# Kernel optimization log

Hardware: AMD Instinct MI355X
Metric: run time of the kernel (lower is better)

Reference implementation:

```python
import jax, jax.numpy as jnp
import numpy as np

N = 768          # number of atoms
DIM = 3
F = 128          # feature width
N_RBF = 32       # gaussian radial basis size
CUTOFF = 5.0
NUM_CHAINS = 4
T_IN_K = 300.0
TTIME = 20.0
KB = 8.617330337217213e-05   # Boltzmann constant, eV/K (ASE units.kB)
BOX = 24.8                   # box side so that ~26 neighbors/atom within cutoff
GAMMA = 1.0 / (CUTOFF / N_RBF) ** 2  # RBF width


def setup_inputs() -> dict:
    key = jax.random.key(0)
    ks = jax.random.split(key, 12)
    q = jax.random.uniform(ks[0], (N, DIM), dtype=jnp.float32) * BOX
    v = jax.random.normal(ks[1], (N, DIM), dtype=jnp.float32) * 0.01
    p_eta = jax.random.normal(ks[2], (NUM_CHAINS,), dtype=jnp.float32) * 0.1
    mass = jax.random.uniform(ks[3], (N,), dtype=jnp.float32, minval=1.0, maxval=20.0)
    atomic_numbers = jax.random.randint(ks[4], (N,), 0, 100, dtype=jnp.int32)
    embed = jax.random.normal(ks[5], (100, F), dtype=jnp.float32) * 0.1
    W1 = jax.random.normal(ks[6], (N_RBF, F), dtype=jnp.float32) / np.sqrt(N_RBF)
    b1 = jnp.zeros((F,), dtype=jnp.float32)
    W2 = jax.random.normal(ks[7], (F, F), dtype=jnp.float32) / np.sqrt(F)
    b2 = jnp.zeros((F,), dtype=jnp.float32)
    W3 = jax.random.normal(ks[8], (F, F), dtype=jnp.float32) / np.sqrt(F)
    w_out = jax.random.normal(ks[9], (F,), dtype=jnp.float32) / np.sqrt(F)
    return dict(v=v, q=q, p_eta=p_eta, mass=mass, embed=embed, W1=W1, b1=b1,
                W2=W2, b2=b2, W3=W3, w_out=w_out, atomic_numbers=atomic_numbers)


def _energy(q, atomic_numbers, embed, W1, b1, W2, b2, W3, w_out):
    """SchNet-style cutoff-graph potential energy (scalar)."""
    h = embed[atomic_numbers]                                   # [N,F]
    disp = q[:, None, :] - q[None, :, :]                        # [N,N,3]
    d2 = jnp.sum(disp * disp, axis=-1)                          # [N,N]
    eye = jnp.eye(N, dtype=bool)
    mask = (d2 < CUTOFF ** 2) & (~eye)                          # cutoff neighbor list (dense mask)
    d = jnp.sqrt(jnp.where(mask, d2, 1.0))                      # safe sqrt off-graph
    centers = jnp.linspace(0.0, CUTOFF, N_RBF, dtype=q.dtype)
    rbf = jnp.exp(-GAMMA * (d[..., None] - centers) ** 2)       # [N,N,n_rbf]
    filt = jax.nn.relu(rbf @ W1 + b1) @ W2 + b2                 # [N,N,F]
    filt = jnp.where(mask[..., None], filt, 0.0)
    m = jnp.einsum('ijf,jf->if', filt, h)                       # message aggregation
    h = h + jax.nn.relu(m @ W3)
    return jnp.sum(h @ w_out)


def reference(v, q, p_eta, mass, embed, W1, b1, W2, b2, W3, w_out, atomic_numbers):
    kT = T_IN_K * KB
    n_dof = N * DIM
    target_ke = 0.5 * n_dof * kT
    Q = 2.0 * jnp.array([n_dof * kT * TTIME ** 2] + [kT * TTIME ** 2] * (NUM_CHAINS - 1),
                        dtype=v.dtype)
    p = v * mass[:, None]                                       # momenta
    current_ke = 0.5 * jnp.sum(p * p / mass[:, None])
    # f = -dE/dq (torch: -results['energy_grad'])
    f = -jax.grad(_energy)(q, atomic_numbers, embed, W1, b1, W2, b2, W3, w_out)
    coupled_forces = (p_eta[0] * p.reshape(-1) / Q[0]).reshape(-1, 3)
    dvdt = (f - coupled_forces) / mass[:, None]
    dpeta_first = 2.0 * (current_ke - target_ke) - p_eta[0] * p_eta[1] / Q[1]
    dpeta_mid = p_eta[:-2] ** 2 / Q[:-2] - kT - p_eta[1:-1] * p_eta[2:] / Q[2:]
    dpeta_last = p_eta[-2] ** 2 / Q[-2] - kT
    dpeta_dt = jnp.concatenate([dpeta_first[None], dpeta_mid, dpeta_last[None]])
    return (dvdt, v, dpeta_dt)
```

## Files before the change

kernel.cpp:

```cpp
#include <hip/hip_runtime.h>
#include <math.h>

#define N_ATOMS 768
#define FD 128
#define NRBF 32
#define MAXN 64
#define NTHREADS 512
#define TST 136
#define RSTU 40

constexpr float  CUT2   = 25.0f;
constexpr float  GAMMA_ = 40.96f;
constexpr float  CSTEP  = 5.0f / 31.0f;
constexpr double KB_D   = 8.617330337217213e-05;
constexpr double KT_D   = 300.0 * KB_D;
constexpr float  KT_F   = (float)KT_D;
constexpr float  TARGET_KE = (float)(0.5 * 2304.0 * KT_D);
constexpr float  Q0_F   = (float)(2.0 * 2304.0 * KT_D * 400.0);
constexpr float  QI_F   = (float)(2.0 * KT_D * 400.0);

#define DVDT_OFF 0
#define V_OFF    (3 * N_ATOMS)
#define PETA_OFF (6 * N_ATOMS)

using short8v = __attribute__((ext_vector_type(8))) short;
using f32x4   = __attribute__((ext_vector_type(4))) float;

#define MFMA_B16 __builtin_amdgcn_mfma_f32_16x16x32_bf16

__device__ __forceinline__ unsigned short f2bf(float x) {
    unsigned int u = __float_as_uint(x);
    u += 0x7FFF + ((u >> 16) & 1);
    return (unsigned short)(u >> 16);
}
__device__ __forceinline__ float bf2f(unsigned short h) {
    return __uint_as_float(((unsigned int)h) << 16);
}


__global__ __launch_bounds__(NTHREADS) void atom_kernel(
    const float* __restrict__ q,
    const float* __restrict__ W1, const float* __restrict__ b1,
    const float* __restrict__ W2, const float* __restrict__ b2,
    const float* __restrict__ embed, const int* __restrict__ z,
    const float* __restrict__ W3, const float* __restrict__ wout,
    float* __restrict__ f_acc)
{
    __shared__ int   nj[MAXN];
    __shared__ float nd[MAXN], ndx[MAXN], ndy[MAXN], ndz[MAXN];
    __shared__ int   cnt_s;
    __shared__ int   z_s[N_ATOMS];
    __shared__ __align__(16) unsigned short poolR[2 * MAXN * RSTU];
    __shared__ __align__(16) unsigned short poolA[2 * MAXN * TST];
    __shared__ float mrow[FD], gb[FD], mbrow[FD];
    __shared__ float sred[8 * MAXN];

    unsigned short* rbf_h  = poolR;
    unsigned short* rbf_l  = poolR + MAXN * RSTU;
    unsigned short* crbf_h = poolR;
    unsigned short* crbf_l = poolR + MAXN * RSTU;
    unsigned short* a1h  = poolA;
    unsigned short* a1l  = poolA + MAXN * TST;
    unsigned short* ts_h = poolA;
    unsigned short* ts_l = poolA + MAXN * TST;

    int i = blockIdx.x, t = threadIdx.x;
    int wid = t >> 6, lane = t & 63;
    int lr = lane & 15, lg = lane >> 4;
    int c0 = wid * 16 + lr;

    if (t == 0) cnt_s = 0;
    __syncthreads();

    float w1f32[8], w2ff32[4][8];
#pragma unroll
    for (int e = 0; e < 8; e++)
        w1f32[e] = W1[(lg * 8 + e) * FD + c0];
#pragma unroll
    for (int ks = 0; ks < 4; ks++)
#pragma unroll
        for (int e = 0; e < 8; e++)
            w2ff32[ks][e] = W2[(ks * 32 + lg * 8 + e) * FD + c0];
    float bb0  = b1[c0];
    float b2c0 = b2[c0];

    float qx = q[i*3], qy = q[i*3+1], qz = q[i*3+2];
    for (int j = t; j < N_ATOMS; j += NTHREADS) {
        z_s[j] = z[j];
        if (j == i) continue;
        float dx = qx - q[j*3], dy = qy - q[j*3+1], dz = qz - q[j*3+2];
        float d2 = dx*dx + dy*dy + dz*dz;
        if (d2 < CUT2) {
            int p = atomicAdd(&cnt_s, 1);
            if (p < MAXN) { nj[p] = j; nd[p] = sqrtf(d2);
                            ndx[p] = dx; ndy[p] = dy; ndz[p] = dz; }
        }
    }
    __syncthreads();
    int cnt = min(cnt_s, MAXN);
    if (cnt == 0) return;
    int ntl = (cnt + 15) >> 4;

    short8v w1h_r, w1l_r, w2f_h[4], w2f_l[4];
#pragma unroll
    for (int e = 0; e < 8; e++) {
        unsigned short hb = f2bf(w1f32[e]);
        w1h_r[e] = (short)hb;
        w1l_r[e] = (short)f2bf(w1f32[e] - bf2f(hb));
    }
#pragma unroll
    for (int ks = 0; ks < 4; ks++)
#pragma unroll
        for (int e = 0; e < 8; e++) {
            unsigned short hb = f2bf(w2ff32[ks][e]);
            w2f_h[ks][e] = (short)hb;
            w2f_l[ks][e] = (short)f2bf(w2ff32[ks][e] - bf2f(hb));
        }

    float macc0 = 0.f;
    unsigned int mk = 0;

    float4 hj0[2];
#pragma unroll
    for (int e = 0; e < 2; e++) {
        int idx = t + e * NTHREADS;
        int p = idx >> 5, c4g = (idx & 31) * 4;
        hj0[e] = (p < cnt)
            ? *(const float4*)(embed + z_s[nj[p]] * FD + c4g)
            : make_float4(0.f, 0.f, 0.f, 0.f);
    }

    for (int e = 0; e < ntl; e++) {
        int idx = t + e * NTHREADS;
        int p = idx >> 5, k = idx & 31;
        float d = (p < cnt) ? nd[p] : 1.0f;
        float u = d - CSTEP * (float)k;
        float r = __expf(-GAMMA_ * u * u);
        unsigned short hb = f2bf(r);
        rbf_h[p * RSTU + k] = hb;
        rbf_l[p * RSTU + k] = f2bf(r - bf2f(hb));
    }
    __syncthreads();

    for (int tl = 0; tl < ntl; tl++) {
        int rb = tl * 16;
        f32x4 u0 = {bb0, bb0, bb0, bb0};
        short8v rh = *(const short8v*)(rbf_h + (rb + lr) * RSTU + lg * 8);
        short8v rl = *(const short8v*)(rbf_l + (rb + lr) * RSTU + lg * 8);
        u0 = MFMA_B16(rh, w1h_r, u0, 0,0,0);
        u0 = MFMA_B16(rh, w1l_r, u0, 0,0,0);
        u0 = MFMA_B16(rl, w1h_r, u0, 0,0,0);
#pragma unroll
        for (int r = 0; r < 4; r++) {
            int p = rb + lg * 4 + r;
            if (u0[r] > 0.f) mk |= 1u << (4 * tl + r);
            float v = fmaxf(u0[r], 0.f);
            unsigned short hb = f2bf(v);
            a1h[p * TST + c0] = hb;
            a1l[p * TST + c0] = f2bf(v - bf2f(hb));
        }
    }
    __syncthreads();

    for (int tl = 0; tl < ntl; tl++) {
        int rb = tl * 16;
        float hv[4];
#pragma unroll
        for (int r = 0; r < 4; r++) {
            int p = rb + lg * 4 + r;
            hv[r] = (p < cnt) ? embed[z_s[nj[p]] * FD + c0] : 0.f;
        }
        f32x4 acc = {0.f, 0.f, 0.f, 0.f};
#pragma unroll
        for (int ks = 0; ks < 4; ks++) {
            int kb = ks * 32 + lg * 8;
            short8v ah = *(const short8v*)(a1h + (rb + lr) * TST + kb);
            short8v al = *(const short8v*)(a1l + (rb + lr) * TST + kb);
            acc = MFMA_B16(ah, w2f_h[ks], acc, 0,0,0);
            acc = MFMA_B16(ah, w2f_l[ks], acc, 0,0,0);
            acc = MFMA_B16(al, w2f_h[ks], acc, 0,0,0);
        }
#pragma unroll
        for (int r = 0; r < 4; r++) macc0 += (acc[r] + b2c0) * hv[r];
    }

    short8v w2b_h[4], w2b_l[4];
#pragma unroll
    for (int ks = 0; ks < 4; ks++) {
        int kb = ks * 32 + lg * 8;
        float4 a = *(const float4*)(W2 + c0 * FD + kb);
        float4 b = *(const float4*)(W2 + c0 * FD + kb + 4);
        float vv[8] = {a.x, a.y, a.z, a.w, b.x, b.y, b.z, b.w};
#pragma unroll
        for (int e = 0; e < 8; e++) {
            unsigned short hb = f2bf(vv[e]);
            w2b_h[ks][e] = (short)hb;
            w2b_l[ks][e] = (short)f2bf(vv[e] - bf2f(hb));
        }
    }

    {
        float r0 = macc0 + __shfl_xor(macc0, 16, 64);
        r0 += __shfl_xor(r0, 32, 64);
        if (lg == 0) mrow[c0] = r0;
    }
    __syncthreads();

    {
        int f0h = lg * 32;
        float g = 0.f;
#pragma unroll 8
        for (int f = f0h; f < f0h + 32; f++)
            g += mrow[f] * W3[f * FD + c0];
        g += __shfl_xor(g, 16, 64);
        g += __shfl_xor(g, 32, 64);
        if (lg == 0) gb[c0] = (g > 0.f) ? wout[c0] : 0.f;
    }
    __syncthreads();
    {
        int f0h = lg * 32;
        float mb = 0.f;
#pragma unroll
        for (int f4 = 0; f4 < 32; f4 += 4) {
            float4 w  = *(const float4*)(W3 + c0 * FD + f0h + f4);
            float4 gv = *(const float4*)(gb + f0h + f4);
            mb += gv.x*w.x + gv.y*w.y + gv.z*w.z + gv.w*w.w;
        }
        mb += __shfl_xor(mb, 16, 64);
        mb += __shfl_xor(mb, 32, 64);
        if (lg == 0) mbrow[c0] = mb;
    }
    __syncthreads();

    for (int e = 0; e < ntl; e++) {
        int idx = t + e * NTHREADS;
        int p = idx >> 5, k = idx & 31;
        float d = (p < cnt) ? nd[p] : 1.0f;
        float u = d - CSTEP * (float)k;
        float r = __expf(-GAMMA_ * u * u);
        float cd = -2.f * GAMMA_ * u * r;
        unsigned short hc = f2bf(cd);
        crbf_h[p * RSTU + k] = hc;
        crbf_l[p * RSTU + k] = f2bf(cd - bf2f(hc));
    }
    for (int e = 0; e < ntl; e++) {
        int idx = t + e * NTHREADS;
        int p = idx >> 5, c4g = (idx & 31) * 4;
        ushort4 hv = {0,0,0,0}, lv = {0,0,0,0};
        if (p < cnt) {
            float4 mb4 = *(const float4*)(mbrow + c4g);
            float4 hj4 = (e < 2) ? hj0[e]
                : *(const float4*)(embed + z_s[nj[p]] * FD + c4g);
            float v0 = mb4.x*hj4.x, v1 = mb4.y*hj4.y;
            float v2 = mb4.z*hj4.z, v3 = mb4.w*hj4.w;
            hv.x = f2bf(v0); lv.x = f2bf(v0 - bf2f(hv.x));
            hv.y = f2bf(v1); lv.y = f2bf(v1 - bf2f(hv.y));
            hv.z = f2bf(v2); lv.z = f2bf(v2 - bf2f(hv.z));
            hv.w = f2bf(v3); lv.w = f2bf(v3 - bf2f(hv.w));
        }
        *(ushort4*)(ts_h + p * TST + c4g) = hv;
        *(ushort4*)(ts_l + p * TST + c4g) = lv;
    }
    __syncthreads();

    for (int tl = 0; tl < ntl; tl++) {
        int rb = tl * 16;
        f32x4 ef = {0.f, 0.f, 0.f, 0.f};
        {
            short8v ch = *(const short8v*)(crbf_h + (rb + lr) * RSTU + lg * 8);
            short8v cl = *(const short8v*)(crbf_l + (rb + lr) * RSTU + lg * 8);
            ef = MFMA_B16(ch, w1h_r, ef, 0,0,0);
            ef = MFMA_B16(ch, w1l_r, ef, 0,0,0);
            ef = MFMA_B16(cl, w1h_r, ef, 0,0,0);
        }
        unsigned int mt = (mk >> (4 * tl)) & 0xFu;
#pragma unroll
        for (int r = 0; r < 4; r++)
            ef[r] = (mt & (1u << r)) ? ef[r] : 0.f;

        f32x4 acc = {0.f, 0.f, 0.f, 0.f};
#pragma unroll
        for (int ks = 0; ks < 4; ks++) {
            int kb = ks * 32 + lg * 8;
            short8v ah = *(const short8v*)(ts_h + (rb + lr) * TST + kb);
            short8v al = *(const short8v*)(ts_l + (rb + lr) * TST + kb);
            acc = MFMA_B16(ah, w2b_h[ks], acc, 0,0,0);
            acc = MFMA_B16(ah, w2b_l[ks], acc, 0,0,0);
            acc = MFMA_B16(al, w2b_h[ks], acc, 0,0,0);
        }

        float p4[4];
#pragma unroll
        for (int r = 0; r < 4; r++) p4[r] = acc[r] * ef[r];
#pragma unroll
        for (int mask = 1; mask < 16; mask <<= 1) {
#pragma unroll
            for (int e = 0; e < 4; e++) p4[e] += __shfl_xor(p4[e], mask, 64);
        }
        if (lr == 0) {
#pragma unroll
            for (int r = 0; r < 4; r++)
                sred[wid * MAXN + rb + lg * 4 + r] = p4[r];
        }
    }
    __syncthreads();

    float iax = 0.f, iay = 0.f, iaz = 0.f;
    if (t < MAXN && t < cnt) {
        float s = 0.f;
#pragma unroll
        for (int w = 0; w < 8; w++) s += sred[w * MAXN + t];
        float coef = s / nd[t];
        float fx = coef * ndx[t];
        float fy = coef * ndy[t];
        float fz = coef * ndz[t];
        iax = fx; iay = fy; iaz = fz;
        atomicAdd(f_acc + nj[t]*3 + 0, fx);
        atomicAdd(f_acc + nj[t]*3 + 1, fy);
        atomicAdd(f_acc + nj[t]*3 + 2, fz);
    }

    if (t < MAXN) {
#pragma unroll
        for (int mask = 1; mask < 64; mask <<= 1) {
            iax += __shfl_xor(iax, mask, 64);
            iay += __shfl_xor(iay, mask, 64);
            iaz += __shfl_xor(iaz, mask, 64);
        }
        if (t == 0) {
            atomicAdd(f_acc + i*3 + 0, -iax);
            atomicAdd(f_acc + i*3 + 1, -iay);
            atomicAdd(f_acc + i*3 + 2, -iaz);
        }
    }
}

__global__ __launch_bounds__(256) void fin_kernel(
    const float* __restrict__ v, const float* __restrict__ mass,
    const float* __restrict__ p_eta, const float* __restrict__ f_acc,
    float* __restrict__ out)
{
    __shared__ float red[256];
    int t = threadIdx.x;
    float ke = 0.f;
    float c = p_eta[0] / Q0_F;
    for (int idx = t; idx < 3 * N_ATOMS; idx += 256) {
        int a = idx / 3;
        float vv = v[idx], mi = mass[a];
        out[DVDT_OFF + idx] = (f_acc[idx] - c * vv * mi) / mi;
        out[V_OFF + idx] = vv;
        ke += 0.5f * mi * vv * vv;
    }
    red[t] = ke;
    __syncthreads();
    for (int s = 128; s > 0; s >>= 1) {
        if (t < s) red[t] += red[t + s];
        __syncthreads();
    }
    if (t == 0) {
        float k0 = red[0];
        float e0 = p_eta[0], e1 = p_eta[1], e2 = p_eta[2], e3 = p_eta[3];
        out[PETA_OFF + 0] = 2.f * (k0 - TARGET_KE) - e0 * e1 / QI_F;
        out[PETA_OFF + 1] = e0 * e0 / Q0_F - KT_F - e1 * e2 / QI_F;
        out[PETA_OFF + 2] = e1 * e1 / QI_F - KT_F - e2 * e3 / QI_F;
        out[PETA_OFF + 3] = e2 * e2 / QI_F - KT_F;
    }
}

extern "C" void kernel_launch(void* const* d_in, const int* in_sizes, int n_in,
                              void* d_out, int out_size, void* d_ws, size_t ws_size,
                              hipStream_t stream)
{
    const float* v     = (const float*)d_in[0];
    const float* q     = (const float*)d_in[1];
    const float* p_eta = (const float*)d_in[2];
    const float* mass  = (const float*)d_in[3];
    const float* embed = (const float*)d_in[4];
    const float* W1    = (const float*)d_in[5];
    const float* b1    = (const float*)d_in[6];
    const float* W2    = (const float*)d_in[7];
    const float* b2    = (const float*)d_in[8];
    const float* W3    = (const float*)d_in[9];
    const float* wout  = (const float*)d_in[10];
    const int*   z     = (const int*)d_in[11];
    float* out = (float*)d_out;

    float* f_acc = (float*)d_ws;

    hipMemsetAsync(f_acc, 0, 3 * N_ATOMS * sizeof(float), stream);

    atom_kernel<<<N_ATOMS, NTHREADS, 0, stream>>>(q, W1, b1, W2, b2,
                                                  embed, z, W3, wout, f_acc);
    fin_kernel<<<1, 256, 0, stream>>>(v, mass, p_eta, f_acc, out);
}
```

Baseline: 117.9 us.

## Process three atoms per block and prefetch next atom's neighbor list

The grid shrinks from one block per atom to 256 persistent blocks, each handling three atoms in sequence. The per-block weight loading and bf16 hi/lo splitting of W1/W2 now happens once for three atoms instead of once per atom. The neighbor search for the next atom runs in double-buffered shared arrays, interleaved with the current atom's work to hide its global loads. In exchange there are fewer blocks (256, roughly the CU count) and less parallelism to hide latency, so each block's three atoms run strictly one after another.

```diff
diff --git a/kernel.cpp b/kernel.cpp
--- a/kernel.cpp
+++ b/kernel.cpp
@@ -6,6 +6,7 @@
 #define NRBF 32
 #define MAXN 64
 #define NTHREADS 512
+#define NBLOCKS 256
 #define TST 136
 #define RSTU 40
 
@@ -46,9 +47,9 @@
     const float* __restrict__ W3, const float* __restrict__ wout,
     float* __restrict__ f_acc)
 {
-    __shared__ int   nj[MAXN];
-    __shared__ float nd[MAXN], ndx[MAXN], ndy[MAXN], ndz[MAXN];
-    __shared__ int   cnt_s;
+    __shared__ int   nj2[2][MAXN];
+    __shared__ float nd2[2][MAXN], ndx2[2][MAXN], ndy2[2][MAXN], ndz2[2][MAXN];
+    __shared__ int   cnt2[2];
     __shared__ int   z_s[N_ATOMS];
     __shared__ __align__(16) unsigned short poolR[2 * MAXN * RSTU];
     __shared__ __align__(16) unsigned short poolA[2 * MAXN * TST];
@@ -64,12 +65,12 @@
     unsigned short* ts_h = poolA;
     unsigned short* ts_l = poolA + MAXN * TST;
 
-    int i = blockIdx.x, t = threadIdx.x;
+    int b = blockIdx.x, t = threadIdx.x;
     int wid = t >> 6, lane = t & 63;
     int lr = lane & 15, lg = lane >> 4;
     int c0 = wid * 16 + lr;
 
-    if (t == 0) cnt_s = 0;
+    if (t < 2) cnt2[t] = 0;
     __syncthreads();
 
     float w1f32[8], w2ff32[4][8];
@@ -84,22 +85,20 @@
     float bb0  = b1[c0];
     float b2c0 = b2[c0];
 
-    float qx = q[i*3], qy = q[i*3+1], qz = q[i*3+2];
-    for (int j = t; j < N_ATOMS; j += NTHREADS) {
-        z_s[j] = z[j];
-        if (j == i) continue;
-        float dx = qx - q[j*3], dy = qy - q[j*3+1], dz = qz - q[j*3+2];
-        float d2 = dx*dx + dy*dy + dz*dz;
-        if (d2 < CUT2) {
-            int p = atomicAdd(&cnt_s, 1);
-            if (p < MAXN) { nj[p] = j; nd[p] = sqrtf(d2);
-                            ndx[p] = dx; ndy[p] = dy; ndz[p] = dz; }
-        }
-    }
-    __syncthreads();
-    int cnt = min(cnt_s, MAXN);
-    if (cnt == 0) return;
-    int ntl = (cnt + 15) >> 4;
+    {
+        float qx = q[b*3], qy = q[b*3+1], qz = q[b*3+2];
+        for (int j = t; j < N_ATOMS; j += NTHREADS) {
+            z_s[j] = z[j];
+            if (j == b) continue;
+            float dx = qx - q[j*3], dy = qy - q[j*3+1], dz = qz - q[j*3+2];
+            float d2 = dx*dx + dy*dy + dz*dz;
+            if (d2 < CUT2) {
+                int p = atomicAdd(&cnt2[0], 1);
+                if (p < MAXN) { nj2[0][p] = j; nd2[0][p] = sqrtf(d2);
+                                ndx2[0][p] = dx; ndy2[0][p] = dy; ndz2[0][p] = dz; }
+            }
+        }
+    }
 
     short8v w1h_r, w1l_r, w2f_h[4], w2f_l[4];
 #pragma unroll
@@ -116,81 +115,13 @@
             w2f_h[ks][e] = (short)hb;
             w2f_l[ks][e] = (short)f2bf(w2ff32[ks][e] - bf2f(hb));
         }
-
-    float macc0 = 0.f;
-    unsigned int mk = 0;
-
-    float4 hj0[2];
-#pragma unroll
-    for (int e = 0; e < 2; e++) {
-        int idx = t + e * NTHREADS;
-        int p = idx >> 5, c4g = (idx & 31) * 4;
-        hj0[e] = (p < cnt)
-            ? *(const float4*)(embed + z_s[nj[p]] * FD + c4g)
-            : make_float4(0.f, 0.f, 0.f, 0.f);
-    }
-
-    for (int e = 0; e < ntl; e++) {
-        int idx = t + e * NTHREADS;
-        int p = idx >> 5, k = idx & 31;
-        float d = (p < cnt) ? nd[p] : 1.0f;
-        float u = d - CSTEP * (float)k;
-        float r = __expf(-GAMMA_ * u * u);
-        unsigned short hb = f2bf(r);
-        rbf_h[p * RSTU + k] = hb;
-        rbf_l[p * RSTU + k] = f2bf(r - bf2f(hb));
-    }
-    __syncthreads();
-
-    for (int tl = 0; tl < ntl; tl++) {
-        int rb = tl * 16;
-        f32x4 u0 = {bb0, bb0, bb0, bb0};
-        short8v rh = *(const short8v*)(rbf_h + (rb + lr) * RSTU + lg * 8);
-        short8v rl = *(const short8v*)(rbf_l + (rb + lr) * RSTU + lg * 8);
-        u0 = MFMA_B16(rh, w1h_r, u0, 0,0,0);
-        u0 = MFMA_B16(rh, w1l_r, u0, 0,0,0);
-        u0 = MFMA_B16(rl, w1h_r, u0, 0,0,0);
-#pragma unroll
-        for (int r = 0; r < 4; r++) {
-            int p = rb + lg * 4 + r;
-            if (u0[r] > 0.f) mk |= 1u << (4 * tl + r);
-            float v = fmaxf(u0[r], 0.f);
-            unsigned short hb = f2bf(v);
-            a1h[p * TST + c0] = hb;
-            a1l[p * TST + c0] = f2bf(v - bf2f(hb));
-        }
-    }
-    __syncthreads();
-
-    for (int tl = 0; tl < ntl; tl++) {
-        int rb = tl * 16;
-        float hv[4];
-#pragma unroll
-        for (int r = 0; r < 4; r++) {
-            int p = rb + lg * 4 + r;
-            hv[r] = (p < cnt) ? embed[z_s[nj[p]] * FD + c0] : 0.f;
-        }
-        f32x4 acc = {0.f, 0.f, 0.f, 0.f};
-#pragma unroll
-        for (int ks = 0; ks < 4; ks++) {
-            int kb = ks * 32 + lg * 8;
-            short8v ah = *(const short8v*)(a1h + (rb + lr) * TST + kb);
-            short8v al = *(const short8v*)(a1l + (rb + lr) * TST + kb);
-            acc = MFMA_B16(ah, w2f_h[ks], acc, 0,0,0);
-            acc = MFMA_B16(ah, w2f_l[ks], acc, 0,0,0);
-            acc = MFMA_B16(al, w2f_h[ks], acc, 0,0,0);
-        }
-#pragma unroll
-        for (int r = 0; r < 4; r++) macc0 += (acc[r] + b2c0) * hv[r];
-    }
-
     short8v w2b_h[4], w2b_l[4];
 #pragma unroll
     for (int ks = 0; ks < 4; ks++) {
         int kb = ks * 32 + lg * 8;
-        float4 a = *(const float4*)(W2 + c0 * FD + kb);
-        float4 b = *(const float4*)(W2 + c0 * FD + kb + 4);
-        float vv[8] = {a.x, a.y, a.z, a.w, b.x, b.y, b.z, b.w};
+        float4 a4 = *(const float4*)(W2 + c0 * FD + kb);
+        float4 b4 = *(const float4*)(W2 + c0 * FD + kb + 4);
+        float vv[8] = {a4.x, a4.y, a4.z, a4.w, b4.x, b4.y, b4.z, b4.w};
 #pragma unroll
         for (int e = 0; e < 8; e++) {
             unsigned short hb = f2bf(vv[e]);
@@ -198,140 +129,236 @@
             w2b_l[ks][e] = (short)f2bf(vv[e] - bf2f(hb));
         }
     }
-
-    {
-        float r0 = macc0 + __shfl_xor(macc0, 16, 64);
-        r0 += __shfl_xor(r0, 32, 64);
-        if (lg == 0) mrow[c0] = r0;
-    }
     __syncthreads();
 
-    {
-        int f0h = lg * 32;
-        float g = 0.f;
+    for (int a = 0; a < 3; a++) {
+        int i   = b + NBLOCKS * a;
+        int buf = a & 1;
+        int nbuf = buf ^ 1;
+        int* njb = nj2[buf];
+        float* ndb = nd2[buf], *ndxb = ndx2[buf], *ndyb = ndy2[buf], *ndzb = ndz2[buf];
+
+        int cnt = min(cnt2[buf], MAXN);
+        int ntl = (cnt + 15) >> 4;
+        if (a < 2 && t == 0) cnt2[nbuf] = 0;
+
+        float macc0 = 0.f;
+        unsigned int mk = 0;
+
+        float4 hj0[2];
+#pragma unroll
+        for (int e = 0; e < 2; e++) {
+            int idx = t + e * NTHREADS;
+            int p = idx >> 5, c4g = (idx & 31) * 4;
+            hj0[e] = (p < cnt)
+                ? *(const float4*)(embed + z_s[njb[p]] * FD + c4g)
+                : make_float4(0.f, 0.f, 0.f, 0.f);
+        }
+
+        for (int e = 0; e < ntl; e++) {
+            int idx = t + e * NTHREADS;
+            int p = idx >> 5, k = idx & 31;
+            float d = (p < cnt) ? ndb[p] : 1.0f;
+            float u = d - CSTEP * (float)k;
+            float r = __expf(-GAMMA_ * u * u);
+            unsigned short hb = f2bf(r);
+            rbf_h[p * RSTU + k] = hb;
+            rbf_l[p * RSTU + k] = f2bf(r - bf2f(hb));
+        }
+        __syncthreads();
+
+        for (int tl = 0; tl < ntl; tl++) {
+            int rb = tl * 16;
+            f32x4 u0 = {bb0, bb0, bb0, bb0};
+            short8v rh = *(const short8v*)(rbf_h + (rb + lr) * RSTU + lg * 8);
+            short8v rl = *(const short8v*)(rbf_l + (rb + lr) * RSTU + lg * 8);
+            u0 = MFMA_B16(rh, w1h_r, u0, 0,0,0);
+            u0 = MFMA_B16(rh, w1l_r, u0, 0,0,0);
+            u0 = MFMA_B16(rl, w1h_r, u0, 0,0,0);
+#pragma unroll
+            for (int r = 0; r < 4; r++) {
+                int p = rb + lg * 4 + r;
+                if (u0[r] > 0.f) mk |= 1u << (4 * tl + r);
+                float v = fmaxf(u0[r], 0.f);
+                unsigned short hb = f2bf(v);
+                a1h[p * TST + c0] = hb;
+                a1l[p * TST + c0] = f2bf(v - bf2f(hb));
+            }
+        }
+        __syncthreads();
+
+        for (int tl = 0; tl < ntl; tl++) {
+            int rb = tl * 16;
+            float hv[4];
+#pragma unroll
+            for (int r = 0; r < 4; r++) {
+                int p = rb + lg * 4 + r;
+                hv[r] = (p < cnt) ? embed[z_s[njb[p]] * FD + c0] : 0.f;
+            }
+            f32x4 acc = {0.f, 0.f, 0.f, 0.f};
+#pragma unroll
+            for (int ks = 0; ks < 4; ks++) {
+                int kb = ks * 32 + lg * 8;
+                short8v ah = *(const short8v*)(a1h + (rb + lr) * TST + kb);
+                short8v al = *(const short8v*)(a1l + (rb + lr) * TST + kb);
+                acc = MFMA_B16(ah, w2f_h[ks], acc, 0,0,0);
+                acc = MFMA_B16(ah, w2f_l[ks], acc, 0,0,0);
+                acc = MFMA_B16(al, w2f_h[ks], acc, 0,0,0);
+            }
+#pragma unroll
+            for (int r = 0; r < 4; r++) macc0 += (acc[r] + b2c0) * hv[r];
+        }
+
+        if (a < 2) {
+            int in = b + NBLOCKS * (a + 1);
+            float qx = q[in*3], qy = q[in*3+1], qz = q[in*3+2];
+            for (int j = t; j < N_ATOMS; j += NTHREADS) {
+                if (j == in) continue;
+                float dx = qx - q[j*3], dy = qy - q[j*3+1], dz = qz - q[j*3+2];
+                float d2 = dx*dx + dy*dy + dz*dz;
+                if (d2 < CUT2) {
+                    int p = atomicAdd(&cnt2[nbuf], 1);
+                    if (p < MAXN) { nj2[nbuf][p] = j; nd2[nbuf][p] = sqrtf(d2);
+                                    ndx2[nbuf][p] = dx; ndy2[nbuf][p] = dy;
+                                    ndz2[nbuf][p] = dz; }
+                }
+            }
+        }
+
+        {
+            float r0 = macc0 + __shfl_xor(macc0, 16, 64);
+            r0 += __shfl_xor(r0, 32, 64);
+            if (lg == 0) mrow[c0] = r0;
+        }
+        __syncthreads();
+
+        {
+            int f0h = lg * 32;
+            float g = 0.f;
 #pragma unroll 8
-        for (int f = f0h; f < f0h + 32; f++)
-            g += mrow[f] * W3[f * FD + c0];
-        g += __shfl_xor(g, 16, 64);
-        g += __shfl_xor(g, 32, 64);
-        if (lg == 0) gb[c0] = (g > 0.f) ? wout[c0] : 0.f;
-    }
-    __syncthreads();
-    {
-        int f0h = lg * 32;
-        float mb = 0.f;
-#pragma unroll
-        for (int f4 = 0; f4 < 32; f4 += 4) {
-            float4 w  = *(const float4*)(W3 + c0 * FD + f0h + f4);
-            float4 gv = *(const float4*)(gb + f0h + f4);
-            mb += gv.x*w.x + gv.y*w.y + gv.z*w.z + gv.w*w.w;
-        }
-        mb += __shfl_xor(mb, 16, 64);
-        mb += __shfl_xor(mb, 32, 64);
-        if (lg == 0) mbrow[c0] = mb;
-    }
-    __syncthreads();
-
-    for (int e = 0; e < ntl; e++) {
-        int idx = t + e * NTHREADS;
-        int p = idx >> 5, k = idx & 31;
-        float d = (p < cnt) ? nd[p] : 1.0f;
-        float u = d - CSTEP * (float)k;
-        float r = __expf(-GAMMA_ * u * u);
-        float cd = -2.f * GAMMA_ * u * r;
-        unsigned short hc = f2bf(cd);
-        crbf_h[p * RSTU + k] = hc;
-        crbf_l[p * RSTU + k] = f2bf(cd - bf2f(hc));
-    }
-    for (int e = 0; e < ntl; e++) {
-        int idx = t + e * NTHREADS;
-        int p = idx >> 5, c4g = (idx & 31) * 4;
-        ushort4 hv = {0,0,0,0}, lv = {0,0,0,0};
-        if (p < cnt) {
-            float4 mb4 = *(const float4*)(mbrow + c4g);
-            float4 hj4 = (e < 2) ? hj0[e]
-                : *(const float4*)(embed + z_s[nj[p]] * FD + c4g);
-            float v0 = mb4.x*hj4.x, v1 = mb4.y*hj4.y;
-            float v2 = mb4.z*hj4.z, v3 = mb4.w*hj4.w;
-            hv.x = f2bf(v0); lv.x = f2bf(v0 - bf2f(hv.x));
-            hv.y = f2bf(v1); lv.y = f2bf(v1 - bf2f(hv.y));
-            hv.z = f2bf(v2); lv.z = f2bf(v2 - bf2f(hv.z));
-            hv.w = f2bf(v3); lv.w = f2bf(v3 - bf2f(hv.w));
-        }
-        *(ushort4*)(ts_h + p * TST + c4g) = hv;
-        *(ushort4*)(ts_l + p * TST + c4g) = lv;
-    }
-    __syncthreads();
-
-    for (int tl = 0; tl < ntl; tl++) {
-        int rb = tl * 16;
-        f32x4 ef = {0.f, 0.f, 0.f, 0.f};
+            for (int f = f0h; f < f0h + 32; f++)
+                g += mrow[f] * W3[f * FD + c0];
+            g += __shfl_xor(g, 16, 64);
+            g += __shfl_xor(g, 32, 64);
+            if (lg == 0) gb[c0] = (g > 0.f) ? wout[c0] : 0.f;
+        }
+        __syncthreads();
         {
-            short8v ch = *(const short8v*)(crbf_h + (rb + lr) * RSTU + lg * 8);
-            short8v cl = *(const short8v*)(crbf_l + (rb + lr) * RSTU + lg * 8);
-            ef = MFMA_B16(ch, w1h_r, ef, 0,0,0);
-            ef = MFMA_B16(ch, w1l_r, ef, 0,0,0);
-            ef = MFMA_B16(cl, w1h_r, ef, 0,0,0);
-        }
-        unsigned int mt = (mk >> (4 * tl)) & 0xFu;
-#pragma unroll
-        for (int r = 0; r < 4; r++)
-            ef[r] = (mt & (1u << r)) ? ef[r] : 0.f;
-
-        f32x4 acc = {0.f, 0.f, 0.f, 0.f};
-#pragma unroll
-        for (int ks = 0; ks < 4; ks++) {
-            int kb = ks * 32 + lg * 8;
-            short8v ah = *(const short8v*)(ts_h + (rb + lr) * TST + kb);
-            short8v al = *(const short8v*)(ts_l + (rb + lr) * TST + kb);
-            acc = MFMA_B16(ah, w2b_h[ks], acc, 0,0,0);
-            acc = MFMA_B16(ah, w2b_l[ks], acc, 0,0,0);
-            acc = MFMA_B16(al, w2b_h[ks], acc, 0,0,0);
-        }
-
-        float p4[4];
-#pragma unroll
-        for (int r = 0; r < 4; r++) p4[r] = acc[r] * ef[r];
-#pragma unroll
-        for (int mask = 1; mask < 16; mask <<= 1) {
-#pragma unroll
-            for (int e = 0; e < 4; e++) p4[e] += __shfl_xor(p4[e], mask, 64);
-        }
-        if (lr == 0) {
+            int f0h = lg * 32;
+            float mb = 0.f;
+#pragma unroll
+            for (int f4 = 0; f4 < 32; f4 += 4) {
+                float4 w  = *(const float4*)(W3 + c0 * FD + f0h + f4);
+                float4 gv = *(const float4*)(gb + f0h + f4);
+                mb += gv.x*w.x + gv.y*w.y + gv.z*w.z + gv.w*w.w;
+            }
+            mb += __shfl_xor(mb, 16, 64);
+            mb += __shfl_xor(mb, 32, 64);
+            if (lg == 0) mbrow[c0] = mb;
+        }
+        __syncthreads();
+
+        for (int e = 0; e < ntl; e++) {
+            int idx = t + e * NTHREADS;
+            int p = idx >> 5, k = idx & 31;
+            float d = (p < cnt) ? ndb[p] : 1.0f;
+            float u = d - CSTEP * (float)k;
+            float r = __expf(-GAMMA_ * u * u);
+            float cd = -2.f * GAMMA_ * u * r;
+            unsigned short hc = f2bf(cd);
+            crbf_h[p * RSTU + k] = hc;
+            crbf_l[p * RSTU + k] = f2bf(cd - bf2f(hc));
+        }
+        for (int e = 0; e < ntl; e++) {
+            int idx = t + e * NTHREADS;
+            int p = idx >> 5, c4g = (idx & 31) * 4;
+            ushort4 hv = {0,0,0,0}, lv = {0,0,0,0};
+            if (p < cnt) {
+                float4 mb4 = *(const float4*)(mbrow + c4g);
+                float4 hj4 = (e < 2) ? hj0[e]
+                    : *(const float4*)(embed + z_s[njb[p]] * FD + c4g);
+                float v0 = mb4.x*hj4.x, v1 = mb4.y*hj4.y;
+                float v2 = mb4.z*hj4.z, v3 = mb4.w*hj4.w;
+                hv.x = f2bf(v0); lv.x = f2bf(v0 - bf2f(hv.x));
+                hv.y = f2bf(v1); lv.y = f2bf(v1 - bf2f(hv.y));
+                hv.z = f2bf(v2); lv.z = f2bf(v2 - bf2f(hv.z));
+                hv.w = f2bf(v3); lv.w = f2bf(v3 - bf2f(hv.w));
+            }
+            *(ushort4*)(ts_h + p * TST + c4g) = hv;
+            *(ushort4*)(ts_l + p * TST + c4g) = lv;
+        }
+        __syncthreads();
+
+        for (int tl = 0; tl < ntl; tl++) {
+            int rb = tl * 16;
+            f32x4 ef = {0.f, 0.f, 0.f, 0.f};
+            {
+                short8v ch = *(const short8v*)(crbf_h + (rb + lr) * RSTU + lg * 8);
+                short8v cl = *(const short8v*)(crbf_l + (rb + lr) * RSTU + lg * 8);
+                ef = MFMA_B16(ch, w1h_r, ef, 0,0,0);
+                ef = MFMA_B16(ch, w1l_r, ef, 0,0,0);
+                ef = MFMA_B16(cl, w1h_r, ef, 0,0,0);
+            }
+            unsigned int mt = (mk >> (4 * tl)) & 0xFu;
 #pragma unroll
             for (int r = 0; r < 4; r++)
-                sred[wid * MAXN + rb + lg * 4 + r] = p4[r];
-        }
-    }
-    __syncthreads();
-
-    float iax = 0.f, iay = 0.f, iaz = 0.f;
-    if (t < MAXN && t < cnt) {
-        float s = 0.f;
-#pragma unroll
-        for (int w = 0; w < 8; w++) s += sred[w * MAXN + t];
-        float coef = s / nd[t];
-        float fx = coef * ndx[t];
-        float fy = coef * ndy[t];
-        float fz = coef * ndz[t];
-        iax = fx; iay = fy; iaz = fz;
-        atomicAdd(f_acc + nj[t]*3 + 0, fx);
-        atomicAdd(f_acc + nj[t]*3 + 1, fy);
-        atomicAdd(f_acc + nj[t]*3 + 2, fz);
-    }
-
-    if (t < MAXN) {
-#pragma unroll
-        for (int mask = 1; mask < 64; mask <<= 1) {
-            iax += __shfl_xor(iax, mask, 64);
-            iay += __shfl_xor(iay, mask, 64);
-            iaz += __shfl_xor(iaz, mask, 64);
-        }
-        if (t == 0) {
-            atomicAdd(f_acc + i*3 + 0, -iax);
-            atomicAdd(f_acc + i*3 + 1, -iay);
-            atomicAdd(f_acc + i*3 + 2, -iaz);
-        }
+                ef[r] = (mt & (1u << r)) ? ef[r] : 0.f;
+
+            f32x4 acc = {0.f, 0.f, 0.f, 0.f};
+#pragma unroll
+            for (int ks = 0; ks < 4; ks++) {
+                int kb = ks * 32 + lg * 8;
+                short8v ah = *(const short8v*)(ts_h + (rb + lr) * TST + kb);
+                short8v al = *(const short8v*)(ts_l + (rb + lr) * TST + kb);
+                acc = MFMA_B16(ah, w2b_h[ks], acc, 0,0,0);
+                acc = MFMA_B16(ah, w2b_l[ks], acc, 0,0,0);
+                acc = MFMA_B16(al, w2b_h[ks], acc, 0,0,0);
+            }
+
+            float p4[4];
+#pragma unroll
+            for (int r = 0; r < 4; r++) p4[r] = acc[r] * ef[r];
+#pragma unroll
+            for (int mask = 1; mask < 16; mask <<= 1) {
+#pragma unroll
+                for (int e = 0; e < 4; e++) p4[e] += __shfl_xor(p4[e], mask, 64);
+            }
+            if (lr == 0) {
+#pragma unroll
+                for (int r = 0; r < 4; r++)
+                    sred[wid * MAXN + rb + lg * 4 + r] = p4[r];
+            }
+        }
+        __syncthreads();
+
+        float iax = 0.f, iay = 0.f, iaz = 0.f;
+        if (t < MAXN && t < cnt) {
+            float s = 0.f;
+#pragma unroll
+            for (int w = 0; w < 8; w++) s += sred[w * MAXN + t];
+            float coef = s / ndb[t];
+            float fx = coef * ndxb[t];
+            float fy = coef * ndyb[t];
+            float fz = coef * ndzb[t];
+            iax = fx; iay = fy; iaz = fz;
+            atomicAdd(f_acc + njb[t]*3 + 0, fx);
+            atomicAdd(f_acc + njb[t]*3 + 1, fy);
+            atomicAdd(f_acc + njb[t]*3 + 2, fz);
+        }
+        if (t < MAXN) {
+#pragma unroll
+            for (int mask = 1; mask < 64; mask <<= 1) {
+                iax += __shfl_xor(iax, mask, 64);
+                iay += __shfl_xor(iay, mask, 64);
+                iaz += __shfl_xor(iaz, mask, 64);
+            }
+            if (t == 0 && cnt > 0) {
+                atomicAdd(f_acc + i*3 + 0, -iax);
+                atomicAdd(f_acc + i*3 + 1, -iay);
+                atomicAdd(f_acc + i*3 + 2, -iaz);
+            }
+        }
+        __syncthreads();
     }
 }
 
@@ -389,7 +416,7 @@
 
     hipMemsetAsync(f_acc, 0, 3 * N_ATOMS * sizeof(float), stream);
 
-    atom_kernel<<<N_ATOMS, NTHREADS, 0, stream>>>(q, W1, b1, W2, b2,
+    atom_kernel<<<NBLOCKS, NTHREADS, 0, stream>>>(q, W1, b1, W2, b2,
                                                   embed, z, W3, wout, f_acc);
     fin_kernel<<<1, 256, 0, stream>>>(v, mass, p_eta, f_acc, out);
 }
```

New measurement: 109.5 us. 7.1% less time.
